# Kernel optimization log

Measured on AMD Instinct MI355X. Metric: run time of the kernel, lower is better.

## Reference

```python
import jax, jax.numpy as jnp
import numpy as np

N_P, N_D = 100000, 50000
C, S, H = 128, 128, 128
E = 600000


def setup_inputs() -> dict:
    key = jax.random.key(0)
    ks = jax.random.split(key, 20)
    sc = 1.0 / np.sqrt(H)
    inp = {
        "h_p": jax.random.normal(ks[0], (N_P, C), dtype=jnp.float32),
        "h_d": jax.random.normal(ks[1], (N_D, S), dtype=jnp.float32),
        "pd_src": jax.random.randint(ks[2], (E,), 0, N_P),
        "pd_dst": jax.random.randint(ks[3], (E,), 0, N_D),
        "dp_src": jax.random.randint(ks[4], (E,), 0, N_D),
        "dp_dst": jax.random.randint(ks[5], (E,), 0, N_P),
    }
    names = [("W1_pd", (C, H)), ("W1_dp", (S, H)), ("W2_pd", (H, H)),
             ("W2_dp", (H, H)), ("W3_pd", (H, S)), ("W3_dp", (H, C))]
    for i, (nm, shp) in enumerate(names):
        inp[nm] = jax.random.normal(ks[6 + i], shp, dtype=jnp.float32) * sc
        inp["b" + nm[1:]] = jnp.zeros((shp[1],), dtype=jnp.float32)
    return inp


def gconv(x, src, dst, n_dst, W, b):
    """DGL GraphConv, norm='both': relu(D_dst^-1/2 A D_src^-1/2 X W + b)."""
    n_src = x.shape[0]
    ones = jnp.ones(src.shape, dtype=x.dtype)
    deg_out = jnp.maximum(jax.ops.segment_sum(ones, src, num_segments=n_src), 1.0)
    deg_in = jnp.maximum(jax.ops.segment_sum(ones, dst, num_segments=n_dst), 1.0)
    xs = x * jax.lax.rsqrt(deg_out)[:, None]
    m = jax.ops.segment_sum(xs[src], dst, num_segments=n_dst)  # [n_dst, d_in]
    m = m * jax.lax.rsqrt(deg_in)[:, None]
    return jax.nn.relu(m @ W + b)


def reference(h_p, h_d, pd_src, pd_dst, dp_src, dp_dst,
              W1_pd, b1_pd, W1_dp, b1_dp,
              W2_pd, b2_pd, W2_dp, b2_dp,
              W3_pd, b3_pd, W3_dp, b3_dp):
    # Layer 1: p_d sends p feats to d; d_p sends d feats to p
    h_d1 = gconv(h_p, pd_src, pd_dst, N_D, W1_pd, b1_pd)
    h_p1 = gconv(h_d, dp_src, dp_dst, N_P, W1_dp, b1_dp)
    # Layer 2
    h_d2 = gconv(h_p1, pd_src, pd_dst, N_D, W2_pd, b2_pd)
    h_p2 = gconv(h_d1, dp_src, dp_dst, N_P, W2_dp, b2_dp)
    # Layer 3: d gets S-dim, p gets C-dim
    h_d3 = gconv(h_p2, pd_src, pd_dst, N_D, W3_pd, b3_pd)
    h_p3 = gconv(h_d2, dp_src, dp_dst, N_P, W3_dp, b3_dp)
    return h_p3, h_d3
```

## Files before the change

kernel.cpp:

```cpp
#include <hip/hip_runtime.h>
#include <stdint.h>

#define N_P 100000
#define N_D 50000
#define NE  600000
#define F   128
#define FP  136

#define NCHK   16
#define CHKE   37504
#define HPH    4
#define HPS    8
#define HOFS_A0 ((size_t)0)
#define HOFS_A1 ((size_t)NCHK*N_P)
#define HOFS_A2 ((size_t)NCHK*N_P + (size_t)NCHK*N_D)
#define HOFS_A3 ((size_t)NCHK*N_P + (size_t)2*NCHK*N_D)

typedef __attribute__((ext_vector_type(8))) __bf16 bf16x8;
typedef __attribute__((ext_vector_type(4))) float  f32x4;

static __device__ __forceinline__ float bf2f(uint16_t u){
  union{float f;uint32_t i;} v; v.i = ((uint32_t)u)<<16; return v.f;
}
static __device__ __forceinline__ uint16_t f2bf(float f){
  union{float f;uint32_t i;} v; v.f = f;
  uint32_t i = v.i;
  uint32_t r = i + 0x7fffu + ((i>>16)&1u);
  return (uint16_t)(r>>16);
}

__global__ __launch_bounds__(512) void k_hist(
    const int* __restrict__ pd_src, const int* __restrict__ pd_dst,
    const int* __restrict__ dp_src, const int* __restrict__ dp_dst,
    int* __restrict__ hist){
  __shared__ uint32_t cnt[(N_P/HPH)/2];
  const int b = blockIdx.x;
  const int arr = b >> 6, part = (b >> 4) & 3, chunk = b & 15;
  const int* src; int N; size_t hofs;
  switch(arr){
    case 0:  src = pd_src; N = N_P; hofs = HOFS_A0; break;
    case 1:  src = pd_dst; N = N_D; hofs = HOFS_A1; break;
    case 2:  src = dp_src; N = N_D; hofs = HOFS_A2; break;
    default: src = dp_dst; N = N_P; hofs = HOFS_A3; break;
  }
  const int PART = N / HPH;
  const int nw   = PART >> 1;
  const int lo   = part * PART;
  for (int i = threadIdx.x; i < nw; i += 512) cnt[i] = 0;
  __syncthreads();
  const int e0 = chunk*CHKE, e1 = min(e0 + CHKE, NE);
  const uint4* s4 = (const uint4*)(src + e0);
  const int n4 = (e1 - e0) >> 2;
  for (int i = threadIdx.x; i < n4; i += 512){
    uint4 v = s4[i];
    int a0 = (int)v.x - lo, a1 = (int)v.y - lo, a2 = (int)v.z - lo, a3 = (int)v.w - lo;
    if ((unsigned)a0 < (unsigned)PART) atomicAdd(&cnt[a0>>1], 1u << ((a0&1)<<4));
    if ((unsigned)a1 < (unsigned)PART) atomicAdd(&cnt[a1>>1], 1u << ((a1&1)<<4));
    if ((unsigned)a2 < (unsigned)PART) atomicAdd(&cnt[a2>>1], 1u << ((a2&1)<<4));
    if ((unsigned)a3 < (unsigned)PART) atomicAdd(&cnt[a3>>1], 1u << ((a3&1)<<4));
  }
  __syncthreads();
  int* out = hist + hofs + (size_t)chunk*N + lo;
  for (int i = threadIdx.x; i < nw; i += 512){
    uint32_t w = cnt[i];
    out[2*i]   = (int)(w & 0xffffu);
    out[2*i+1] = (int)(w >> 16);
  }
}

__global__ void k_sumdeg(int* __restrict__ hist,
                         int* __restrict__ cnt_d_in, int* __restrict__ cnt_p_in,
                         float* __restrict__ rs_p_out, float* __restrict__ rs_p_in,
                         float* __restrict__ rs_d_out, float* __restrict__ rs_d_in){
  const int idx = blockIdx.x*256 + threadIdx.x;
  const int arr = blockIdx.y;
  int N; size_t hofs; bool pre;
  switch(arr){
    case 0:  N = N_P; hofs = HOFS_A0; pre = false; break;
    case 1:  N = N_D; hofs = HOFS_A1; pre = true;  break;
    case 2:  N = N_D; hofs = HOFS_A2; pre = false; break;
    default: N = N_P; hofs = HOFS_A3; pre = true;  break;
  }
  if (idx >= N) return;
  int* base = hist + hofs + idx;
  int run = 0;
  if (pre){
    #pragma unroll 4
    for (int c = 0; c < NCHK; ++c){
      int v = base[(size_t)c*N]; base[(size_t)c*N] = run; run += v;
    }
  } else {
    #pragma unroll 4
    for (int c = 0; c < NCHK; ++c) run += base[(size_t)c*N];
  }
  float rs = rsqrtf((float)max(run, 1));
  switch(arr){
    case 0:  rs_p_out[idx] = rs; break;
    case 1:  cnt_d_in[idx] = run; rs_d_in[idx] = rs; break;
    case 2:  rs_d_out[idx] = rs; break;
    default: cnt_p_in[idx] = run; rs_p_in[idx] = rs; break;
  }
}

__global__ void k_scan1(const int* __restrict__ cA, int nA,
                        const int* __restrict__ cB, int nB,
                        int* __restrict__ bsums, int nbA){
  __shared__ int red[8];
  int b = blockIdx.x, t = threadIdx.x;
  const int* in; int n, bi, slot;
  if (b < nbA){ in = cA; n = nA; bi = b;       slot = bi; }
  else        { in = cB; n = nB; bi = b - nbA; slot = 256 + bi; }
  int i = bi*512 + t;
  int v = (i < n) ? in[i] : 0;
  #pragma unroll
  for (int o = 32; o; o >>= 1) v += __shfl_down(v, o, 64);
  if ((t & 63) == 0) red[t >> 6] = v;
  __syncthreads();
  if (t == 0){ int s = 0; for (int k = 0; k < 8; ++k) s += red[k]; bsums[slot] = s; }
}

__global__ void k_scan2(int* bsums, int nbA, int nbB){
  __shared__ int sh[256];
  int seg = blockIdx.x, t = threadIdx.x;
  int nb = seg ? nbB : nbA;
  int* p = bsums + seg*256;
  int v = (t < nb) ? p[t] : 0;
  sh[t] = v; __syncthreads();
  for (int ofs = 1; ofs < 256; ofs <<= 1){
    int u = (t >= ofs) ? sh[t-ofs] : 0; __syncthreads();
    sh[t] += u; __syncthreads();
  }
  if (t < nb) p[t] = sh[t] - v;
}

__global__ void k_scan3(const int* __restrict__ cA, int nA,
                        const int* __restrict__ cB, int nB,
                        const int* __restrict__ bsums, int nbA,
                        int* __restrict__ offA, int* __restrict__ offB){
  __shared__ int sh[512];
  int b = blockIdx.x, t = threadIdx.x;
  const int* in; int n, bi; int* out; int base;
  if (b < nbA){ in = cA; n = nA; bi = b;       out = offA; base = bsums[bi]; }
  else        { in = cB; n = nB; bi = b - nbA; out = offB; base = bsums[256+bi]; }
  int i = bi*512 + t;
  int v = (i < n) ? in[i] : 0;
  sh[t] = v; __syncthreads();
  for (int ofs = 1; ofs < 512; ofs <<= 1){
    int u = (t >= ofs) ? sh[t-ofs] : 0; __syncthreads();
    sh[t] += u; __syncthreads();
  }
  if (i < n) out[i] = base + sh[t] - v;
  if (b == 0 && t == 0){ offA[nA] = NE; offB[nB] = NE; }
}

__global__ __launch_bounds__(512) void k_scatter(
    const int* __restrict__ pd_src, const int* __restrict__ pd_dst,
    const int* __restrict__ dp_src, const int* __restrict__ dp_dst,
    const int* __restrict__ off_pd, const int* __restrict__ off_dp,
    const int* __restrict__ hist,
    int* __restrict__ col_pd, int* __restrict__ col_dp){
  __shared__ int base[N_P/HPS];
  const int b = blockIdx.x;
  const int gph = b >> 7, part = (b >> 4) & 7, chunk = b & 15;
  const int* dsts; const int* srcs; const int* off; int* col; int N; size_t hofs;
  if (gph == 0){ dsts = pd_dst; srcs = pd_src; off = off_pd; col = col_pd; N = N_D; hofs = HOFS_A1; }
  else         { dsts = dp_dst; srcs = dp_src; off = off_dp; col = col_dp; N = N_P; hofs = HOFS_A3; }
  const int PART = N / HPS;
  const int lo = part * PART;
  const int* hc   = hist + hofs + (size_t)chunk*N + lo;
  const int* offp = off + lo;
  for (int i = threadIdx.x; i < PART; i += 512) base[i] = offp[i] + hc[i];
  __syncthreads();
  const int e0 = chunk*CHKE, e1 = min(e0 + CHKE, NE);
  const uint4* d4 = (const uint4*)(dsts + e0);
  const int n4 = (e1 - e0) >> 2;
  for (int i = threadIdx.x; i < n4; i += 512){
    uint4 d = d4[i];
    int a0 = (int)d.x - lo, a1 = (int)d.y - lo, a2 = (int)d.z - lo, a3 = (int)d.w - lo;
    int e = e0 + 4*i;
    if ((unsigned)a0 < (unsigned)PART){ int p = atomicAdd(&base[a0], 1); col[p] = srcs[e+0]; }
    if ((unsigned)a1 < (unsigned)PART){ int p = atomicAdd(&base[a1], 1); col[p] = srcs[e+1]; }
    if ((unsigned)a2 < (unsigned)PART){ int p = atomicAdd(&base[a2], 1); col[p] = srcs[e+2]; }
    if ((unsigned)a3 < (unsigned)PART){ int p = atomicAdd(&base[a3], 1); col[p] = srcs[e+3]; }
  }
}

__global__ void k_convert(const float4* __restrict__ hp, const float4* __restrict__ hd,
                          const float* __restrict__ rs_po, const float* __restrict__ rs_do,
                          uint2* __restrict__ P0, uint2* __restrict__ D0,
                          const float* w0,const float* w1,const float* w2,
                          const float* w3,const float* w4,const float* w5,
                          uint16_t* __restrict__ wt,
                          uint16_t* z0, uint16_t* z1, uint16_t* z2,
                          uint16_t* z3, uint16_t* z4, uint16_t* z5){
  if (blockIdx.x < 6){
    int m = blockIdx.x;
    const float* W; uint16_t* Z;
    switch(m){ case 0:W=w0;Z=z0;break; case 1:W=w1;Z=z1;break; case 2:W=w2;Z=z2;break;
               case 3:W=w3;Z=z3;break; case 4:W=w4;Z=z4;break; default:W=w5;Z=z5; }
    uint16_t* T = wt + m*F*FP;
    for (int idx = threadIdx.x; idx < F*F; idx += 256){
      int k = idx >> 7, j = idx & 127;
      T[j*FP + k] = f2bf(W[idx]);
    }
    if (threadIdx.x < F) Z[threadIdx.x] = 0;
    return;
  }
  int i = (blockIdx.x - 6)*256 + threadIdx.x;
  const int nP4 = N_P*F/4, nD4 = N_D*F/4;
  if (i < nP4){
    float4 v = hp[i]; float s = rs_po[i >> 5];
    uint2 r;
    r.x = ((uint32_t)f2bf(v.y*s)<<16) | f2bf(v.x*s);
    r.y = ((uint32_t)f2bf(v.w*s)<<16) | f2bf(v.z*s);
    P0[i] = r;
  } else {
    int j = i - nP4;
    if (j < nD4){
      float4 v = hd[j]; float s = rs_do[j >> 5];
      uint2 r;
      r.x = ((uint32_t)f2bf(v.y*s)<<16) | f2bf(v.x*s);
      r.y = ((uint32_t)f2bf(v.w*s)<<16) | f2bf(v.z*s);
      D0[j] = r;
    }
  }
}

template<int OUT_MODE>
__global__ __launch_bounds__(256, 4) void k_gconv2(
    const uint16_t* __restrict__ xA, const int* __restrict__ offAp, const int* __restrict__ colA,
    const float* __restrict__ rsA, const uint16_t* __restrict__ WtA, const float* __restrict__ biasA,
    const float* __restrict__ rsnA, void* __restrict__ outA, int ndA, int nsA, int nblkA,
    const uint16_t* __restrict__ xB, const int* __restrict__ offBp, const int* __restrict__ colB,
    const float* __restrict__ rsB, const uint16_t* __restrict__ WtB, const float* __restrict__ biasB,
    const float* __restrict__ rsnB, void* __restrict__ outB, int ndB, int nsB)
{
  __shared__ uint16_t m_lds[64*FP];
  const int tid  = threadIdx.x;
  const int lane = tid & 63;
  const int wv   = tid >> 6;

  const uint16_t* x; const int* off; const int* col; const float* rs_in;
  const uint16_t* Wt; const float* bias; const float* rs_next; void* outp;
  int n_dst, zrow, bid;
  if ((int)blockIdx.x < nblkA){
    x = xA; off = offAp; col = colA; rs_in = rsA; Wt = WtA; bias = biasA;
    rs_next = rsnA; outp = outA; n_dst = ndA; zrow = nsA; bid = blockIdx.x;
  } else {
    x = xB; off = offBp; col = colB; rs_in = rsB; Wt = WtB; bias = biasB;
    rs_next = rsnB; outp = outB; n_dst = ndB; zrow = nsB; bid = blockIdx.x - nblkA;
  }

  const int row0 = bid*64 + wv*16;
  const int g    = lane >> 4;
  const int l    = lane & 15;
  const uint16_t* xl = x + l*8;

  int e0a[4], e1a[4], cva[4];
  #pragma unroll
  for (int i = 0; i < 4; ++i){
    int r = row0 + i*4 + g;
    bool rv = r < n_dst;
    e0a[i] = rv ? off[r]   : 0;
    e1a[i] = rv ? off[r+1] : 0;
  }
  #pragma unroll
  for (int i = 0; i < 4; ++i){
    int last = (e1a[i] > 0) ? e1a[i]-1 : 0;
    int idx  = e0a[i] + l;
    cva[i] = col[idx < e1a[i] ? idx : last];
  }

  #pragma unroll
  for (int i = 0; i < 4; ++i){
    int e0 = e0a[i], e1 = e1a[i];
    int cv = cva[i];
    float a0=0.f,a1=0.f,a2=0.f,a3=0.f,a4=0.f,a5=0.f,a6=0.f,a7=0.f;
    for (int e = e0; e < e1; e += 16){
      int nidx = e + 16 + l;
      int ncv  = col[nidx < e1 ? nidx : e1-1];
      int cnt  = e1 - e;
      const bool more = (cnt > 8);
      int cb[16];
      #pragma unroll
      for (int q = 0; q < 8; ++q) cb[q] = __shfl(cv, g*16 + q, 64);
      if (more){
        #pragma unroll
        for (int q = 8; q < 16; ++q) cb[q] = __shfl(cv, g*16 + q, 64);
      }
      uint4 u[8], w[8];
      #pragma unroll
      for (int q = 0; q < 8; ++q){
        int c = (q < cnt) ? cb[q] : zrow;
        u[q] = *(const uint4*)(xl + (size_t)c*F);
      }
      if (more){
        #pragma unroll
        for (int q = 8; q < 16; ++q){
          int c = (q < cnt) ? cb[q] : zrow;
          w[q-8] = *(const uint4*)(xl + (size_t)c*F);
        }
      }
      #pragma unroll
      for (int q = 0; q < 8; ++q){
        a0 += bf2f((uint16_t)u[q].x); a1 += bf2f((uint16_t)(u[q].x>>16));
        a2 += bf2f((uint16_t)u[q].y); a3 += bf2f((uint16_t)(u[q].y>>16));
        a4 += bf2f((uint16_t)u[q].z); a5 += bf2f((uint16_t)(u[q].z>>16));
        a6 += bf2f((uint16_t)u[q].w); a7 += bf2f((uint16_t)(u[q].w>>16));
      }
      if (more){
        #pragma unroll
        for (int q = 0; q < 8; ++q){
          a0 += bf2f((uint16_t)w[q].x); a1 += bf2f((uint16_t)(w[q].x>>16));
          a2 += bf2f((uint16_t)w[q].y); a3 += bf2f((uint16_t)(w[q].y>>16));
          a4 += bf2f((uint16_t)w[q].z); a5 += bf2f((uint16_t)(w[q].z>>16));
          a6 += bf2f((uint16_t)w[q].w); a7 += bf2f((uint16_t)(w[q].w>>16));
        }
      }
      cv = ncv;
    }
    int r = row0 + i*4 + g;
    float rs = (r < n_dst) ? rs_in[r] : 0.f;
    uint4 pk;
    pk.x = ((uint32_t)f2bf(a1*rs)<<16) | f2bf(a0*rs);
    pk.y = ((uint32_t)f2bf(a3*rs)<<16) | f2bf(a2*rs);
    pk.z = ((uint32_t)f2bf(a5*rs)<<16) | f2bf(a4*rs);
    pk.w = ((uint32_t)f2bf(a7*rs)<<16) | f2bf(a6*rs);
    *(uint4*)&m_lds[(wv*16 + i*4 + g)*FP + l*8] = pk;
  }

  f32x4 acc[8];
  #pragma unroll
  for (int t = 0; t < 8; ++t) acc[t] = (f32x4){0.f,0.f,0.f,0.f};
  const int mrow = lane & 15;
  const int kgrp = lane >> 4;
  #pragma unroll
  for (int k0 = 0; k0 < F; k0 += 32){
    bf16x8 bfrag = *(const bf16x8*)&m_lds[(wv*16 + mrow)*FP + k0 + kgrp*8];
    #pragma unroll
    for (int t = 0; t < 8; ++t){
      bf16x8 afrag = *(const bf16x8*)&Wt[(t*16 + mrow)*FP + k0 + kgrp*8];
      acc[t] = __builtin_amdgcn_mfma_f32_16x16x32_bf16(afrag, bfrag, acc[t], 0, 0, 0);
    }
  }

  const int q4 = kgrp * 4;
  const int rr = row0 + mrow;
  if (rr < n_dst){
    float rsn = (OUT_MODE == 0) ? rs_next[rr] : 1.f;
    #pragma unroll
    for (int t = 0; t < 8; ++t){
      float4 b4 = *(const float4*)&bias[t*16 + q4];
      float v0 = fmaxf(acc[t][0] + b4.x, 0.f);
      float v1 = fmaxf(acc[t][1] + b4.y, 0.f);
      float v2 = fmaxf(acc[t][2] + b4.z, 0.f);
      float v3 = fmaxf(acc[t][3] + b4.w, 0.f);
      if (OUT_MODE == 0){
        uint2 pk;
        pk.x = ((uint32_t)f2bf(v1*rsn)<<16) | f2bf(v0*rsn);
        pk.y = ((uint32_t)f2bf(v3*rsn)<<16) | f2bf(v2*rsn);
        *(uint2*)((uint16_t*)outp + (size_t)rr*F + t*16 + q4) = pk;
      } else {
        float4 o; o.x = v0; o.y = v1; o.z = v2; o.w = v3;
        *(float4*)((float*)outp + (size_t)rr*F + t*16 + q4) = o;
      }
    }
  }
}

extern "C" void kernel_launch(void* const* d_in, const int* in_sizes, int n_in,
                              void* d_out, int out_size, void* d_ws, size_t ws_size,
                              hipStream_t stream) {
  const float* h_p   = (const float*)d_in[0];
  const float* h_d   = (const float*)d_in[1];
  const int* pd_src  = (const int*)d_in[2];
  const int* pd_dst  = (const int*)d_in[3];
  const int* dp_src  = (const int*)d_in[4];
  const int* dp_dst  = (const int*)d_in[5];
  const float* W1_pd = (const float*)d_in[6];   const float* b1_pd = (const float*)d_in[7];
  const float* W1_dp = (const float*)d_in[8];   const float* b1_dp = (const float*)d_in[9];
  const float* W2_pd = (const float*)d_in[10];  const float* b2_pd = (const float*)d_in[11];
  const float* W2_dp = (const float*)d_in[12];  const float* b2_dp = (const float*)d_in[13];
  const float* W3_pd = (const float*)d_in[14];  const float* b3_pd = (const float*)d_in[15];
  const float* W3_dp = (const float*)d_in[16];  const float* b3_dp = (const float*)d_in[17];

  char* w = (char*)d_ws;
  size_t o = 0;
  auto take = [&](size_t bytes)->char*{
    char* p = w + o; o += (bytes + 255) & ~(size_t)255; return p;
  };

  int* cnt_d_in  = (int*)take(4*(size_t)N_D);
  int* cnt_p_in  = (int*)take(4*(size_t)N_P);
  int* off_pd   = (int*)take(4*(size_t)(N_D+1));
  int* off_dp   = (int*)take(4*(size_t)(N_P+1));
  int* bsums    = (int*)take(4*512);
  int* col_pd   = (int*)take(4*(size_t)NE);
  int* col_dp   = (int*)take(4*(size_t)NE);
  float* rs_p_out = (float*)take(4*(size_t)N_P);
  float* rs_p_in  = (float*)take(4*(size_t)N_P);
  float* rs_d_out = (float*)take(4*(size_t)N_D);
  float* rs_d_in  = (float*)take(4*(size_t)N_D);
  uint16_t* wt  = (uint16_t*)take(2*(size_t)6*F*FP);
  uint16_t* P0  = (uint16_t*)take(2*(size_t)(N_P+1)*F);
  uint16_t* P1  = (uint16_t*)take(2*(size_t)(N_P+1)*F);
  uint16_t* P2  = (uint16_t*)take(2*(size_t)(N_P+1)*F);
  uint16_t* D0  = (uint16_t*)take(2*(size_t)(N_D+1)*F);
  uint16_t* D1  = (uint16_t*)take(2*(size_t)(N_D+1)*F);
  uint16_t* D2  = (uint16_t*)take(2*(size_t)(N_D+1)*F);

  int* hist = (int*)P1;

  k_hist<<<4*HPH*NCHK, 512, 0, stream>>>(pd_src, pd_dst, dp_src, dp_dst, hist);
  k_sumdeg<<<dim3((N_P+255)/256, 4), 256, 0, stream>>>(
      hist, cnt_d_in, cnt_p_in, rs_p_out, rs_p_in, rs_d_out, rs_d_in);
  const int nbA = (N_D + 511)/512;
  const int nbB = (N_P + 511)/512;
  k_scan1<<<nbA+nbB, 512, 0, stream>>>(cnt_d_in, N_D, cnt_p_in, N_P, bsums, nbA);
  k_scan2<<<2, 256, 0, stream>>>(bsums, nbA, nbB);
  k_scan3<<<nbA+nbB, 512, 0, stream>>>(cnt_d_in, N_D, cnt_p_in, N_P, bsums, nbA, off_pd, off_dp);
  k_scatter<<<2*HPS*NCHK, 512, 0, stream>>>(pd_src, pd_dst, dp_src, dp_dst,
                                            off_pd, off_dp, hist, col_pd, col_dp);
  k_convert<<<((N_P+N_D)*F/4 + 255)/256 + 6, 256, 0, stream>>>(
      (const float4*)h_p, (const float4*)h_d, rs_p_out, rs_d_out, (uint2*)P0, (uint2*)D0,
      W1_pd, W1_dp, W2_pd, W2_dp, W3_pd, W3_dp, wt,
      P0 + (size_t)N_P*F, D0 + (size_t)N_D*F,
      P1 + (size_t)N_P*F, D1 + (size_t)N_D*F,
      P2 + (size_t)N_P*F, D2 + (size_t)N_D*F);

  const int gd = (N_D + 63)/64, gp = (N_P + 63)/64;
  k_gconv2<0><<<gd+gp, 256, 0, stream>>>(
      P0, off_pd, col_pd, rs_d_in, wt + 0*F*FP, b1_pd, rs_d_out, D1, N_D, N_P, gd,
      D0, off_dp, col_dp, rs_p_in, wt + 1*F*FP, b1_dp, rs_p_out, P1, N_P, N_D);
  k_gconv2<0><<<gd+gp, 256, 0, stream>>>(
      P1, off_pd, col_pd, rs_d_in, wt + 2*F*FP, b2_pd, rs_d_out, D2, N_D, N_P, gd,
      D1, off_dp, col_dp, rs_p_in, wt + 3*F*FP, b2_dp, rs_p_out, P2, N_P, N_D);
  k_gconv2<1><<<gd+gp, 256, 0, stream>>>(
      P2, off_pd, col_pd, rs_d_in, wt + 4*F*FP, b3_pd, nullptr, (float*)d_out + (size_t)N_P*F, N_D, N_P, gd,
      D2, off_dp, col_dp, rs_p_in, wt + 5*F*FP, b3_dp, nullptr, (float*)d_out, N_P, N_D);
}
```

Measured before the change: 446.9 us.

## Pack histogram as 16-bit counts, double chunks, use nontemporal gathers and LDS-staged stores

Stores per-chunk degree histograms as packed 16-bit pairs instead of 32-bit ints, which halves histogram traffic, and doubles the number of edge chunks for more parallelism in the hist and scatter kernels. The degree-sum kernel now handles two nodes per thread over one flattened grid. The gather loads in the graph-conv kernel become nontemporal, and the bf16 layer output is staged through LDS so the global stores are wider and coalesced. The risks are extra LDS round-trips in the epilogue and 16-bit count overflow if a chunk ever has very high degree.

```diff
diff --git a/kernel.cpp b/kernel.cpp
--- a/kernel.cpp
+++ b/kernel.cpp
@@ -7,17 +7,19 @@
 #define F   128
 #define FP  136
 
-#define NCHK   16
-#define CHKE   37504
+#define NCHK   32
+#define CHKE   18752
 #define HPH    4
 #define HPS    8
 #define HOFS_A0 ((size_t)0)
 #define HOFS_A1 ((size_t)NCHK*N_P)
 #define HOFS_A2 ((size_t)NCHK*N_P + (size_t)NCHK*N_D)
 #define HOFS_A3 ((size_t)NCHK*N_P + (size_t)2*NCHK*N_D)
+#define CVT_TOT (6 + (N_P+N_D)*F/4/256)
 
 typedef __attribute__((ext_vector_type(8))) __bf16 bf16x8;
 typedef __attribute__((ext_vector_type(4))) float  f32x4;
+typedef unsigned int __attribute__((ext_vector_type(4))) u32x4;
 
 static __device__ __forceinline__ float bf2f(uint16_t u){
   union{float f;uint32_t i;} v; v.i = ((uint32_t)u)<<16; return v.f;
@@ -28,14 +30,18 @@
   uint32_t r = i + 0x7fffu + ((i>>16)&1u);
   return (uint16_t)(r>>16);
 }
+static __device__ __forceinline__ uint4 ld_nt_u4(const uint16_t* p){
+  u32x4 v = __builtin_nontemporal_load((const u32x4*)p);
+  uint4 r; r.x = v.x; r.y = v.y; r.z = v.z; r.w = v.w; return r;
+}
 
 __global__ __launch_bounds__(512) void k_hist(
     const int* __restrict__ pd_src, const int* __restrict__ pd_dst,
     const int* __restrict__ dp_src, const int* __restrict__ dp_dst,
-    int* __restrict__ hist){
+    uint16_t* __restrict__ hist){
   __shared__ uint32_t cnt[(N_P/HPH)/2];
   const int b = blockIdx.x;
-  const int arr = b >> 6, part = (b >> 4) & 3, chunk = b & 15;
+  const int arr = b >> 7, part = (b >> 5) & 3, chunk = b & 31;
   const int* src; int N; size_t hofs;
   switch(arr){
     case 0:  src = pd_src; N = N_P; hofs = HOFS_A0; break;
@@ -60,20 +66,22 @@
     if ((unsigned)a3 < (unsigned)PART) atomicAdd(&cnt[a3>>1], 1u << ((a3&1)<<4));
   }
   __syncthreads();
-  int* out = hist + hofs + (size_t)chunk*N + lo;
-  for (int i = threadIdx.x; i < nw; i += 512){
-    uint32_t w = cnt[i];
-    out[2*i]   = (int)(w & 0xffffu);
-    out[2*i+1] = (int)(w >> 16);
-  }
-}
-
-__global__ void k_sumdeg(int* __restrict__ hist,
-                         int* __restrict__ cnt_d_in, int* __restrict__ cnt_p_in,
-                         float* __restrict__ rs_p_out, float* __restrict__ rs_p_in,
-                         float* __restrict__ rs_d_out, float* __restrict__ rs_d_in){
-  const int idx = blockIdx.x*256 + threadIdx.x;
-  const int arr = blockIdx.y;
+  uint32_t* out32 = (uint32_t*)(hist + hofs + (size_t)chunk*N + lo);
+  for (int i = threadIdx.x; i < nw; i += 512) out32[i] = cnt[i];
+}
+
+__global__ __launch_bounds__(512) void k_sumdeg(
+    uint16_t* __restrict__ hist,
+    int* __restrict__ cnt_d_in, int* __restrict__ cnt_p_in,
+    float* __restrict__ rs_p_out, float* __restrict__ rs_p_in,
+    float* __restrict__ rs_d_out, float* __restrict__ rs_d_in){
+  const int gid = blockIdx.x*512 + threadIdx.x;
+  if (gid >= (N_P + N_D)) return;
+  int arr, pidx;
+  if      (gid < N_P/2)        { arr = 0; pidx = gid; }
+  else if (gid < N_P/2+N_D/2)  { arr = 1; pidx = gid - N_P/2; }
+  else if (gid < N_P/2+N_D)    { arr = 2; pidx = gid - N_P/2 - N_D/2; }
+  else                         { arr = 3; pidx = gid - N_P/2 - N_D; }
   int N; size_t hofs; bool pre;
   switch(arr){
     case 0:  N = N_P; hofs = HOFS_A0; pre = false; break;
@@ -81,24 +89,33 @@
     case 2:  N = N_D; hofs = HOFS_A2; pre = false; break;
     default: N = N_P; hofs = HOFS_A3; pre = true;  break;
   }
-  if (idx >= N) return;
-  int* base = hist + hofs + idx;
-  int run = 0;
+  uint32_t* h32 = (uint32_t*)(hist + hofs) + pidx;
+  const int stride = N >> 1;
+  int run0 = 0, run1 = 0;
   if (pre){
     #pragma unroll 4
     for (int c = 0; c < NCHK; ++c){
-      int v = base[(size_t)c*N]; base[(size_t)c*N] = run; run += v;
+      uint32_t w = h32[(size_t)c*stride];
+      h32[(size_t)c*stride] = (uint32_t)run0 | ((uint32_t)run1 << 16);
+      run0 += (int)(w & 0xffffu); run1 += (int)(w >> 16);
     }
   } else {
     #pragma unroll 4
-    for (int c = 0; c < NCHK; ++c) run += base[(size_t)c*N];
-  }
-  float rs = rsqrtf((float)max(run, 1));
+    for (int c = 0; c < NCHK; ++c){
+      uint32_t w = h32[(size_t)c*stride];
+      run0 += (int)(w & 0xffffu); run1 += (int)(w >> 16);
+    }
+  }
+  const int idx = 2*pidx;
+  float rs0 = rsqrtf((float)max(run0, 1));
+  float rs1 = rsqrtf((float)max(run1, 1));
   switch(arr){
-    case 0:  rs_p_out[idx] = rs; break;
-    case 1:  cnt_d_in[idx] = run; rs_d_in[idx] = rs; break;
-    case 2:  rs_d_out[idx] = rs; break;
-    default: cnt_p_in[idx] = run; rs_p_in[idx] = rs; break;
+    case 0:  rs_p_out[idx] = rs0; rs_p_out[idx+1] = rs1; break;
+    case 1:  cnt_d_in[idx] = run0; cnt_d_in[idx+1] = run1;
+             rs_d_in[idx] = rs0;  rs_d_in[idx+1] = rs1;  break;
+    case 2:  rs_d_out[idx] = rs0; rs_d_out[idx+1] = rs1; break;
+    default: cnt_p_in[idx] = run0; cnt_p_in[idx+1] = run1;
+             rs_p_in[idx] = rs0;  rs_p_in[idx+1] = rs1;  break;
   }
 }
 
@@ -157,19 +174,23 @@
     const int* __restrict__ pd_src, const int* __restrict__ pd_dst,
     const int* __restrict__ dp_src, const int* __restrict__ dp_dst,
     const int* __restrict__ off_pd, const int* __restrict__ off_dp,
-    const int* __restrict__ hist,
+    const uint16_t* __restrict__ hist,
     int* __restrict__ col_pd, int* __restrict__ col_dp){
   __shared__ int base[N_P/HPS];
   const int b = blockIdx.x;
-  const int gph = b >> 7, part = (b >> 4) & 7, chunk = b & 15;
+  const int gph = b >> 8, part = (b >> 5) & 7, chunk = b & 31;
   const int* dsts; const int* srcs; const int* off; int* col; int N; size_t hofs;
   if (gph == 0){ dsts = pd_dst; srcs = pd_src; off = off_pd; col = col_pd; N = N_D; hofs = HOFS_A1; }
   else         { dsts = dp_dst; srcs = dp_src; off = off_dp; col = col_dp; N = N_P; hofs = HOFS_A3; }
   const int PART = N / HPS;
   const int lo = part * PART;
-  const int* hc   = hist + hofs + (size_t)chunk*N + lo;
+  const uint32_t* hc32 = (const uint32_t*)(hist + hofs + (size_t)chunk*N + lo);
   const int* offp = off + lo;
-  for (int i = threadIdx.x; i < PART; i += 512) base[i] = offp[i] + hc[i];
+  for (int i = threadIdx.x; i < (PART>>1); i += 512){
+    uint32_t w = hc32[i];
+    base[2*i]   = offp[2*i]   + (int)(w & 0xffffu);
+    base[2*i+1] = offp[2*i+1] + (int)(w >> 16);
+  }
   __syncthreads();
   const int e0 = chunk*CHKE, e1 = min(e0 + CHKE, NE);
   const uint4* d4 = (const uint4*)(dsts + e0);
@@ -292,13 +313,13 @@
       #pragma unroll
       for (int q = 0; q < 8; ++q){
         int c = (q < cnt) ? cb[q] : zrow;
-        u[q] = *(const uint4*)(xl + (size_t)c*F);
+        u[q] = ld_nt_u4(xl + (size_t)c*F);
       }
       if (more){
         #pragma unroll
         for (int q = 8; q < 16; ++q){
           int c = (q < cnt) ? cb[q] : zrow;
-          w[q-8] = *(const uint4*)(xl + (size_t)c*F);
+          w[q-8] = ld_nt_u4(xl + (size_t)c*F);
         }
       }
       #pragma unroll
@@ -346,22 +367,41 @@
 
   const int q4 = kgrp * 4;
   const int rr = row0 + mrow;
-  if (rr < n_dst){
-    float rsn = (OUT_MODE == 0) ? rs_next[rr] : 1.f;
+  if (OUT_MODE == 0){
+    float rsn = (rr < n_dst) ? rs_next[rr] : 0.f;
     #pragma unroll
     for (int t = 0; t < 8; ++t){
       float4 b4 = *(const float4*)&bias[t*16 + q4];
-      float v0 = fmaxf(acc[t][0] + b4.x, 0.f);
-      float v1 = fmaxf(acc[t][1] + b4.y, 0.f);
-      float v2 = fmaxf(acc[t][2] + b4.z, 0.f);
-      float v3 = fmaxf(acc[t][3] + b4.w, 0.f);
-      if (OUT_MODE == 0){
-        uint2 pk;
-        pk.x = ((uint32_t)f2bf(v1*rsn)<<16) | f2bf(v0*rsn);
-        pk.y = ((uint32_t)f2bf(v3*rsn)<<16) | f2bf(v2*rsn);
-        *(uint2*)((uint16_t*)outp + (size_t)rr*F + t*16 + q4) = pk;
-      } else {
-        float4 o; o.x = v0; o.y = v1; o.z = v2; o.w = v3;
+      float v0 = fmaxf(acc[t][0] + b4.x, 0.f) * rsn;
+      float v1 = fmaxf(acc[t][1] + b4.y, 0.f) * rsn;
+      float v2 = fmaxf(acc[t][2] + b4.z, 0.f) * rsn;
+      float v3 = fmaxf(acc[t][3] + b4.w, 0.f) * rsn;
+      uint2 pk;
+      pk.x = ((uint32_t)f2bf(v1)<<16) | f2bf(v0);
+      pk.y = ((uint32_t)f2bf(v3)<<16) | f2bf(v2);
+      *(uint2*)&m_lds[(wv*16 + mrow)*FP + t*16 + q4] = pk;
+    }
+    uint16_t* outg = (uint16_t*)outp;
+    const int lr = lane & 15;
+    const int lw = lane >> 4;
+    #pragma unroll
+    for (int it = 0; it < 4; ++it){
+      int rowi = row0 + it*4 + lw;
+      if (rowi < n_dst){
+        uint4 vv = *(const uint4*)&m_lds[(wv*16 + it*4 + lw)*FP + lr*8];
+        *(uint4*)&outg[(size_t)rowi*F + lr*8] = vv;
+      }
+    }
+  } else {
+    if (rr < n_dst){
+      #pragma unroll
+      for (int t = 0; t < 8; ++t){
+        float4 b4 = *(const float4*)&bias[t*16 + q4];
+        float4 o;
+        o.x = fmaxf(acc[t][0] + b4.x, 0.f);
+        o.y = fmaxf(acc[t][1] + b4.y, 0.f);
+        o.z = fmaxf(acc[t][2] + b4.z, 0.f);
+        o.w = fmaxf(acc[t][3] + b4.w, 0.f);
         *(float4*)((float*)outp + (size_t)rr*F + t*16 + q4) = o;
       }
     }
@@ -409,10 +449,10 @@
   uint16_t* D1  = (uint16_t*)take(2*(size_t)(N_D+1)*F);
   uint16_t* D2  = (uint16_t*)take(2*(size_t)(N_D+1)*F);
 
-  int* hist = (int*)P1;
+  uint16_t* hist = P1;
 
   k_hist<<<4*HPH*NCHK, 512, 0, stream>>>(pd_src, pd_dst, dp_src, dp_dst, hist);
-  k_sumdeg<<<dim3((N_P+255)/256, 4), 256, 0, stream>>>(
+  k_sumdeg<<<((N_P+N_D) + 511)/512, 512, 0, stream>>>(
       hist, cnt_d_in, cnt_p_in, rs_p_out, rs_p_in, rs_d_out, rs_d_in);
   const int nbA = (N_D + 511)/512;
   const int nbB = (N_P + 511)/512;
@@ -421,7 +461,7 @@
   k_scan3<<<nbA+nbB, 512, 0, stream>>>(cnt_d_in, N_D, cnt_p_in, N_P, bsums, nbA, off_pd, off_dp);
   k_scatter<<<2*HPS*NCHK, 512, 0, stream>>>(pd_src, pd_dst, dp_src, dp_dst,
                                             off_pd, off_dp, hist, col_pd, col_dp);
-  k_convert<<<((N_P+N_D)*F/4 + 255)/256 + 6, 256, 0, stream>>>(
+  k_convert<<<CVT_TOT, 256, 0, stream>>>(
       (const float4*)h_p, (const float4*)h_d, rs_p_out, rs_d_out, (uint2*)P0, (uint2*)D0,
       W1_pd, W1_dp, W2_pd, W2_dp, W3_pd, W3_dp, wt,
       P0 + (size_t)N_P*F, D0 + (size_t)N_D*F,
```

After: 504.8 us. 1.13x slower.
